# Performance work log

Hardware: AMD Instinct MI355X
Metric: run time of the kernel (lower is better)

The kernel has to match this reference:

```python
import jax, jax.numpy as jnp
import numpy as np

GRID_SIZE = 5   # efficient-kan default
K = 3           # spline_order
BATCH = 32768
OBS_DIM = 128
ACTION_DIM = 18
# (in_features, out_features) for the 7 KANLinear layers:
# base: 128->256->256->64 ; adv head: 64->64->18 ; value head: 64->64->1
DIMS = [(OBS_DIM, 256), (256, 256), (256, 64), (64, 64), (64, ACTION_DIM), (64, 64), (64, 1)]


def make_grid(in_f):
    # uniform grid on [-1,1] extended by K knots each side: shape (in_f, GRID_SIZE+2K+1)
    h = 2.0 / GRID_SIZE
    g = jnp.arange(-K, GRID_SIZE + K + 1, dtype=jnp.float32) * h - 1.0
    return jnp.broadcast_to(g, (in_f, g.shape[0]))


def b_splines(x, grid):
    # Cox-de Boor recursion; x: (B, in) -> bases (B, in, GRID_SIZE+K)
    xe = x[:, :, None]
    b = ((xe >= grid[:, :-1]) & (xe < grid[:, 1:])).astype(x.dtype)
    for j in range(1, K + 1):
        left = (xe - grid[:, : -(j + 1)]) / (grid[:, j:-1] - grid[:, : -(j + 1)])
        right = (grid[:, j + 1:] - xe) / (grid[:, j + 1:] - grid[:, 1:-j])
        b = left * b[:, :, :-1] + right * b[:, :, 1:]
    return b


def kan_layer(x, bw, sw, sc):
    # efficient-kan KANLinear: silu base path + spline path with standalone scaler
    grid = make_grid(x.shape[1])
    base = jax.nn.silu(x) @ bw.T                              # (B, out)
    bases = b_splines(x, grid)                                # (B, in, G+K)
    spline = jnp.einsum('big,oig->bo', bases, sw * sc[:, :, None])
    return base + spline


def setup_inputs() -> dict:
    key = jax.random.key(0)
    ks = jax.random.split(key, 1 + 3 * len(DIMS))
    inp = {"x": jax.random.normal(ks[0], (BATCH, OBS_DIM), dtype=jnp.float32)}
    for i, (fin, fout) in enumerate(DIMS):
        inp[f"bw{i}"] = jax.random.normal(ks[1 + 3 * i], (fout, fin), dtype=jnp.float32) / np.sqrt(fin).astype(np.float32)
        inp[f"sw{i}"] = jax.random.normal(ks[2 + 3 * i], (fout, fin, GRID_SIZE + K), dtype=jnp.float32) * (0.1 / np.sqrt(fin).astype(np.float32))
        inp[f"sc{i}"] = 1.0 + 0.1 * jax.random.normal(ks[3 + 3 * i], (fout, fin), dtype=jnp.float32)
    return inp


def reference(x, bw0, sw0, sc0, bw1, sw1, sc1, bw2, sw2, sc2,
              bw3, sw3, sc3, bw4, sw4, sc4, bw5, sw5, sc5, bw6, sw6, sc6):
    h = x
    for bw, sw, sc in [(bw0, sw0, sc0), (bw1, sw1, sc1), (bw2, sw2, sc2)]:
        h = kan_layer(h, bw, sw, sc)
    advantage = kan_layer(kan_layer(h, bw3, sw3, sc3), bw4, sw4, sc4)
    state_value = kan_layer(kan_layer(h, bw5, sw5, sc5), bw6, sw6, sc6)
    return (advantage, state_value)
```

## Files before the change

### kernel.cpp

```cpp
#include <hip/hip_runtime.h>

typedef unsigned short u16;
typedef unsigned int   u32;
typedef unsigned long long u64;
typedef __bf16 bf16;
typedef float f32x4  __attribute__((ext_vector_type(4)));
typedef bf16  bf16x8 __attribute__((ext_vector_type(8)));

__device__ __forceinline__ float bf2f(u16 u){ return (float)__builtin_bit_cast(bf16,u); }
__device__ __forceinline__ u16   f2bf(float f){ return __builtin_bit_cast(u16,(bf16)f); }
__device__ __forceinline__ u32   pkbf(float a,float b){ return (u32)f2bf(a)|((u32)f2bf(b)<<16); }

#define NROWS 32768

__device__ __forceinline__ void expand_vals(float x, u32& spk, uint4& bpk)
{
  float s = x * (1.0f/(1.0f+__expf(-x)));
  u16 uh = f2bf(s);
  u16 ul = f2bf(s - bf2f(uh));
  spk = (u32)uh | ((u32)ul<<16);
  float tp = __fmaf_rn(x, 2.5f, 5.5f);
  float fi = floorf(tp);
  float uu = tp - fi;
  float u2=uu*uu, u3=u2*uu, w1=1.0f-uu;
  const float c6 = 0.16666666666666666f;
  float d0 = w1*w1*w1*c6;
  float d1 = (4.0f-6.0f*u2+3.0f*u3)*c6;
  float d2 = (1.0f+3.0f*uu+3.0f*u2-3.0f*u3)*c6;
  float d3 = u3*c6;
  u64 dpk = (u64)pkbf(d0,d1) | ((u64)pkbf(d2,d3)<<32);
  int i0 = (int)fminf(fmaxf(fi,-20.f),20.f);
  int ss = (i0-3)*16;
  u64 A  = dpk << (ss & 63);
  u64 Bv = dpk >> ((64-ss) & 63);
  u64 Cv = dpk << ((ss-64) & 63);
  u64 Dv = dpk >> ((-ss) & 63);
  u64 lo = (ss>=0 && ss<64) ? A : ((ss<0 && ss>-64) ? Dv : 0ull);
  u64 hi = (ss>=64 && ss<128) ? Cv : ((ss>0 && ss<64) ? Bv : 0ull);
  bpk.x=(u32)lo; bpk.y=(u32)(lo>>32); bpk.z=(u32)hi; bpk.w=(u32)(hi>>32);
}

struct PrepArgs {
  const float* bw[7]; const float* sw[7]; const float* sc[7];
  u16* w[7];
  int cin[7]; int coutr[7]; int ntsh[7];
  u32 elems[7];
};

__global__ __launch_bounds__(256) void prep_kernel(PrepArgs pa)
{
  u32 idx = blockIdx.x*256 + threadIdx.x;
  int L = 0;
  u32 off = idx;
  while (L < 6 && off >= pa.elems[L]) { off -= pa.elems[L]; ++L; }
  int j    = off & 7;
  int lane = (off>>3) & 63;
  u32 tl   = off >> 9;
  int ntsh = pa.ntsh[L];
  u32 kstep = tl >> ntsh;
  int ntile = (int)(tl & ((1u<<ntsh)-1u));
  int o    = ntile*16 + (lane&15);
  int kpos = (lane>>4)*8 + j;
  u32 c = kstep / 5u;
  int r = (int)(kstep - c*5u);
  int i, g; bool sil;
  if (r == 0){ i = (int)c*16 + (kpos>>1);          g = 0;        sil = true;  }
  else       { int kl=(r-1)*32+kpos; i=(int)c*16+(kl>>3); g=kl&7; sil = false; }
  float v = 0.f;
  if (o < pa.coutr[L]) {
    size_t e = (size_t)o*pa.cin[L] + i;
    v = sil ? pa.bw[L][e] : pa.sw[L][e*8+g]*pa.sc[L][e];
  }
  pa.w[L][off] = f2bf(v);
}

template<int CIN,int COUT,int IN_MODE,int OUT_MODE>
__global__ __launch_bounds__(512,4) void kan_layer(const void* __restrict__ hin_,
    const u16* __restrict__ W, void* __restrict__ hout_)
{
  constexpr int NCH = CIN/16;
  constexpr int TOTK = NCH*5;
  constexpr int NTILES = COUT/16;
  constexpr int NT = (COUT>=128)? COUT/128 : 1;
  constexpr int SROW=20, BROW=68, BOFF=64*SROW;
  constexpr int CHUNK = BOFF + 64*BROW;
  __shared__ u32 buf[2][CHUNK];

  const int b0 = blockIdx.x*64;
  const int tid = threadIdx.x;
  const int wave = tid>>6, lane = tid&63, m = lane&15, quad = lane>>4;

  const u16*   __restrict__ hb = (const u16*)hin_;
  const float* __restrict__ hf = (const float*)hin_;

  f32x4 acc[4][NT];
#pragma unroll
  for (int a=0;a<4;++a)
#pragma unroll
    for (int n=0;n<NT;++n) acc[a][n]=(f32x4){0.f,0.f,0.f,0.f};

  bf16x8 bbuf[3][NT];
  auto loadB = [&](int kstep, bf16x8* dst){
    if (kstep < TOTK){
#pragma unroll
      for (int nt=0; nt<NT; ++nt)
        dst[nt] = *(const bf16x8*)(W + (((size_t)kstep*NTILES + ((wave*NT+nt)&(NTILES-1)))*64 + lane)*8);
    }
  };
  loadB(0, bbuf[0]); loadB(1, bbuf[1]);

  float xb[2][2];
  auto loadX = [&](int kc, float* dst){
#pragma unroll
    for (int t=0;t<2;++t){
      int task = t*512+tid, row = task>>4, f = task&15;
      int gi = (b0+row)*CIN + kc*16 + f;
      dst[t] = (IN_MODE==0)? hf[gi] : bf2f(hb[gi]);
    }
  };
  auto expandChunk = [&](const float* xc, u32* dstb){
#pragma unroll
    for (int t=0;t<2;++t){
      int task=t*512+tid, row=task>>4, f=task&15;
      u32 spk; uint4 bpk;
      expand_vals(xc[t], spk, bpk);
      dstb[row*SROW + f] = spk;
      *(uint4*)&dstb[BOFF + row*BROW + f*4] = bpk;
    }
  };

  loadX(0, xb[0]);
  expandChunk(xb[0], buf[0]);
  loadX(1, xb[1]);
  __syncthreads();

  for (int kc=0; kc<NCH; ++kc){
    u32* cur = buf[kc&1];
    u32* nxt = buf[(kc+1)&1];
    if (kc+1 < NCH) expandChunk(xb[(kc+1)&1], nxt);
    if (kc+2 < NCH) loadX(kc+2, xb[kc&1]);
#pragma unroll
    for (int ks=0; ks<5; ++ks){
      const int kstep = kc*5 + ks;
      loadB(kstep+2, bbuf[2]);
      bf16x8 af[4];
#pragma unroll
      for (int mt=0; mt<4; ++mt){
        int row = mt*16 + m;
        af[mt] = (ks==0)
          ? *(const bf16x8*)&cur[row*SROW + quad*4]
          : *(const bf16x8*)&cur[BOFF + row*BROW + (ks-1)*16 + quad*4];
      }
#pragma unroll
      for (int nt=0; nt<NT; ++nt)
#pragma unroll
        for (int mt=0; mt<4; ++mt)
          acc[mt][nt] = __builtin_amdgcn_mfma_f32_16x16x32_bf16(af[mt], bbuf[0][nt], acc[mt][nt],0,0,0);
#pragma unroll
      for (int nt=0; nt<NT; ++nt){ bbuf[0][nt]=bbuf[1][nt]; bbuf[1][nt]=bbuf[2][nt]; }
    }
    __syncthreads();
  }

  if (wave*NT < NTILES){
#pragma unroll
    for (int mt=0; mt<4; ++mt)
#pragma unroll
      for (int nt=0; nt<NT; ++nt)
#pragma unroll
        for (int r=0; r<4; ++r){
          size_t off = (size_t)(b0 + mt*16 + quad*4 + r)*COUT + ((wave*NT+nt)&(NTILES-1))*16 + m;
          if constexpr (OUT_MODE==0) ((float*)hout_)[off] = acc[mt][nt][r];
          else                       ((u16*)hout_)[off]   = f2bf(acc[mt][nt][r]);
        }
  }
}

template<int IN_MODE>
__global__ __launch_bounds__(512,4) void tail_kernel(const void* __restrict__ h2_,
  const u16* __restrict__ W3, const u16* __restrict__ W4,
  const u16* __restrict__ W5, const u16* __restrict__ W6,
  float* __restrict__ out_adv, float* __restrict__ out_val)
{
  constexpr int SROW=20, BROW=68, BOFF=64*20;
  __shared__ u32   Aexp[BOFF + 64*BROW];
  __shared__ float hA[64*65], hV[64*65];

  const int b0 = blockIdx.x*64;
  const int tid = threadIdx.x;
  const int wave = tid>>6, lane = tid&63, m = lane&15, quad = lane>>4;
  const int rg = wave>>2, cg = wave&3;

  const u16*   __restrict__ hb = (const u16*)h2_;
  const float* __restrict__ hf = (const float*)h2_;

  f32x4 a3[2], a5[2];
#pragma unroll
  for (int mt=0;mt<2;++mt){ a3[mt]=(f32x4){0,0,0,0}; a5[mt]=(f32x4){0,0,0,0}; }

  bf16x8 w3b[3], w5b[3];
  auto loadB2 = [&](int kstep, int d){
    if (kstep < 20){
      size_t bi = (((size_t)kstep*4 + cg)*64 + lane)*8;
      w3b[d] = *(const bf16x8*)(W3+bi);
      w5b[d] = *(const bf16x8*)(W5+bi);
    }
  };
  loadB2(0,0); loadB2(1,1);

  float xb[2][2];
  auto loadX = [&](int kc, float* dst){
#pragma unroll
    for (int t=0;t<2;++t){
      int task = t*512+tid, row=task>>4, f=task&15;
      int gi = (b0+row)*64 + kc*16 + f;
      dst[t] = (IN_MODE==0)? hf[gi] : bf2f(hb[gi]);
    }
  };
  loadX(0, xb[0]);

  for (int kc=0; kc<4; ++kc){
    const float* xc = xb[kc&1];
#pragma unroll
    for (int t=0;t<2;++t){
      int task=t*512+tid, row=task>>4, f=task&15;
      u32 spk; uint4 bpk;
      expand_vals(xc[t], spk, bpk);
      Aexp[row*SROW + f] = spk;
      *(uint4*)&Aexp[BOFF + row*BROW + f*4] = bpk;
    }
    if (kc+1 < 4) loadX(kc+1, xb[(kc+1)&1]);
    __syncthreads();
#pragma unroll
    for (int ks=0; ks<5; ++ks){
      const int kstep = kc*5 + ks;
      loadB2(kstep+2, 2);
      bf16x8 af[2];
#pragma unroll
      for (int mt=0; mt<2; ++mt){
        int row = rg*32 + mt*16 + m;
        af[mt] = (ks==0)
          ? *(const bf16x8*)&Aexp[row*SROW + quad*4]
          : *(const bf16x8*)&Aexp[BOFF + row*BROW + (ks-1)*16 + quad*4];
      }
#pragma unroll
      for (int mt=0; mt<2; ++mt){
        a3[mt] = __builtin_amdgcn_mfma_f32_16x16x32_bf16(af[mt], w3b[0], a3[mt],0,0,0);
        a5[mt] = __builtin_amdgcn_mfma_f32_16x16x32_bf16(af[mt], w5b[0], a5[mt],0,0,0);
      }
      w3b[0]=w3b[1]; w3b[1]=w3b[2]; w5b[0]=w5b[1]; w5b[1]=w5b[2];
    }
    __syncthreads();
  }
#pragma unroll
  for (int mt=0;mt<2;++mt)
#pragma unroll
    for (int r=0;r<4;++r){
      int row = rg*32 + mt*16 + quad*4 + r;
      hA[row*65 + cg*16 + m] = a3[mt][r];
      hV[row*65 + cg*16 + m] = a5[mt][r];
    }
  __syncthreads();

  f32x4 a4[2];
#pragma unroll
  for (int mt=0;mt<2;++mt) a4[mt]=(f32x4){0,0,0,0};
  bf16x8 w4b[3];
  auto loadB4 = [&](int kstep, int d){
    if (kstep < 20) w4b[d] = *(const bf16x8*)(W4 + (((size_t)kstep*4 + cg)*64 + lane)*8);
  };
  loadB4(0,0); loadB4(1,1);
  for (int kc=0; kc<4; ++kc){
#pragma unroll
    for (int t=0;t<2;++t){
      int task=t*512+tid, row=task>>4, f=task&15;
      u32 spk; uint4 bpk;
      expand_vals(hA[row*65 + kc*16 + f], spk, bpk);
      Aexp[row*SROW + f] = spk;
      *(uint4*)&Aexp[BOFF + row*BROW + f*4] = bpk;
    }
    __syncthreads();
#pragma unroll
    for (int ks=0; ks<5; ++ks){
      loadB4(kc*5+ks+2, 2);
      bf16x8 af[2];
#pragma unroll
      for (int mt=0; mt<2; ++mt){
        int row = rg*32 + mt*16 + m;
        af[mt] = (ks==0)
          ? *(const bf16x8*)&Aexp[row*SROW + quad*4]
          : *(const bf16x8*)&Aexp[BOFF + row*BROW + (ks-1)*16 + quad*4];
      }
#pragma unroll
      for (int mt=0; mt<2; ++mt)
        a4[mt] = __builtin_amdgcn_mfma_f32_16x16x32_bf16(af[mt], w4b[0], a4[mt],0,0,0);
      w4b[0]=w4b[1]; w4b[1]=w4b[2];
    }
    __syncthreads();
  }
  {
    int col = cg*16 + m;
    if (col < 18){
#pragma unroll
      for (int mt=0;mt<2;++mt)
#pragma unroll
        for (int r=0;r<4;++r)
          out_adv[(size_t)(b0 + rg*32 + mt*16 + quad*4 + r)*18 + col] = a4[mt][r];
    }
  }

  f32x4 a6[2];
#pragma unroll
  for (int mt=0;mt<2;++mt) a6[mt]=(f32x4){0,0,0,0};
  bf16x8 w6b[3];
  auto loadB6 = [&](int kstep, int d){
    if (kstep < 20) w6b[d] = *(const bf16x8*)(W6 + (((size_t)kstep*4 + cg)*64 + lane)*8);
  };
  loadB6(0,0); loadB6(1,1);
  for (int kc=0; kc<4; ++kc){
#pragma unroll
    for (int t=0;t<2;++t){
      int task=t*512+tid, row=task>>4, f=task&15;
      u32 spk; uint4 bpk;
      expand_vals(hV[row*65 + kc*16 + f], spk, bpk);
      Aexp[row*SROW + f] = spk;
      *(uint4*)&Aexp[BOFF + row*BROW + f*4] = bpk;
    }
    __syncthreads();
#pragma unroll
    for (int ks=0; ks<5; ++ks){
      loadB6(kc*5+ks+2, 2);
      bf16x8 af[2];
#pragma unroll
      for (int mt=0; mt<2; ++mt){
        int row = rg*32 + mt*16 + m;
        af[mt] = (ks==0)
          ? *(const bf16x8*)&Aexp[row*SROW + quad*4]
          : *(const bf16x8*)&Aexp[BOFF + row*BROW + (ks-1)*16 + quad*4];
      }
#pragma unroll
      for (int mt=0; mt<2; ++mt)
        a6[mt] = __builtin_amdgcn_mfma_f32_16x16x32_bf16(af[mt], w6b[0], a6[mt],0,0,0);
      w6b[0]=w6b[1]; w6b[1]=w6b[2];
    }
    __syncthreads();
  }
  if (cg==0 && m==0){
#pragma unroll
    for (int mt=0;mt<2;++mt)
#pragma unroll
      for (int r=0;r<4;++r)
        out_val[b0 + rg*32 + mt*16 + quad*4 + r] = a6[mt][r];
  }
}

extern "C" void kernel_launch(void* const* d_in, const int* in_sizes, int n_in,
                              void* d_out, int out_size, void* d_ws, size_t ws_size,
                              hipStream_t stream)
{
  (void)in_sizes; (void)n_in; (void)out_size;
  char* ws = (char*)d_ws;

  const size_t wbytes[7] = {655360u, 1310720u, 327680u, 81920u, 81920u, 81920u, 81920u};
  const bool midf32 = ws_size >= 78118912u;

  u16* W[7];
  char *h0, *h1, *h2;
  if (midf32) {
    h0 = ws;
    h1 = h0 + 33554432u;
    h2 = h1 + 33554432u;
    size_t off = 75497472u;
    for (int l=0;l<7;++l){ W[l] = (u16*)(ws+off); off += wbytes[l]; }
  } else {
    h0 = ws;
    h1 = h0 + 16777216u;
    h2 = h1 + 16777216u;
    size_t off = 37748736u;
    for (int l=0;l<7;++l){ W[l] = (u16*)(ws+off); off += wbytes[l]; }
  }

  PrepArgs pa;
  const int cins[7]   = {128,256,256,64,64,64,64};
  const int coutr[7]  = {256,256,64,64,18,64,1};
  const int ntsh[7]   = {4,4,2,2,2,2,2};
  const u32 elems[7]  = {327680u,655360u,163840u,40960u,40960u,40960u,40960u};
  for (int l=0;l<7;++l){
    pa.bw[l] = (const float*)d_in[1+3*l];
    pa.sw[l] = (const float*)d_in[2+3*l];
    pa.sc[l] = (const float*)d_in[3+3*l];
    pa.w[l]  = W[l];
    pa.cin[l]=cins[l]; pa.coutr[l]=coutr[l]; pa.ntsh[l]=ntsh[l];
    pa.elems[l]=elems[l];
  }
  prep_kernel<<<5120, 256, 0, stream>>>(pa);

  dim3 g(NROWS/64), b(512);
  float* out_adv = (float*)d_out;
  float* out_val = (float*)d_out + (size_t)NROWS*18;
  if (midf32) {
    kan_layer<128,256,0,0><<<g,b,0,stream>>>(d_in[0], W[0], h0);
    kan_layer<256,256,0,0><<<g,b,0,stream>>>(h0, W[1], h1);
    kan_layer<256, 64,0,0><<<g,b,0,stream>>>(h1, W[2], h2);
    tail_kernel<0><<<g,b,0,stream>>>(h2, W[3], W[4], W[5], W[6], out_adv, out_val);
  } else {
    kan_layer<128,256,0,1><<<g,b,0,stream>>>(d_in[0], W[0], h0);
    kan_layer<256,256,1,1><<<g,b,0,stream>>>(h0, W[1], h1);
    kan_layer<256, 64,1,1><<<g,b,0,stream>>>(h1, W[2], h2);
    tail_kernel<1><<<g,b,0,stream>>>(h2, W[3], W[4], W[5], W[6], out_adv, out_val);
  }
}
```

Before: 238.7 us.

## Drop split-bf16 silu term in main layers to shrink K from 10 to 9 per input

The three main KAN layers previously stored silu as a hi/lo bf16 pair, giving 10 K-columns per input feature (2 silu plus 8 spline). They now keep a single bf16 silu value and process 32 input features per chunk, so K drops to 9 per feature and there are fewer MFMA steps. The 1/6 spline constant moves into the prepped weights, and the cubic basis is computed with fewer operations by clamping tp before the floor. The cost is lower silu precision in the main layers, and the larger LDS buffer (BROW 132) may reduce occupancy.

```diff
diff --git a/kernel.cpp b/kernel.cpp
--- a/kernel.cpp
+++ b/kernel.cpp
@@ -13,37 +13,47 @@
 
 #define NROWS 32768
 
-__device__ __forceinline__ void expand_vals(float x, u32& spk, uint4& bpk)
+__device__ __forceinline__ uint4 basis_pk(float x)
+{
+  float tp  = __fmaf_rn(x, 2.5f, 5.5f);
+  float tpc = fminf(fmaxf(tp, -1.0f), 12.0f);
+  float fi  = floorf(tpc);
+  float uu  = tpc - fi;
+  int   i0  = (int)fi;
+  float u2 = uu*uu, u3 = u2*uu, w1 = 1.0f-uu, w2 = w1*w1, w3 = w2*w1;
+  float d1 = __fmaf_rn(3.0f, u3, __fmaf_rn(-6.0f, u2, 4.0f));
+  float d2 = __fmaf_rn(3.0f, w3, __fmaf_rn(-6.0f, w2, 4.0f));
+  u64 dpk = (u64)pkbf(w3, d1) | ((u64)pkbf(d2, u3) << 32);
+  int ss = i0*16 - 48;
+  u64 A  = dpk << (ss & 63);
+  u64 Bv = dpk >> ((64-ss) & 63);
+  u64 Cv = dpk << ((ss-64) & 63);
+  u64 Dv = dpk >> ((-ss) & 63);
+  u64 lo = (ss>=0 && ss<64)   ? A  : ((ss<0 && ss>-64) ? Dv : 0ull);
+  u64 hi = (ss>=64 && ss<128) ? Cv : ((ss>0 && ss<64)  ? Bv : 0ull);
+  uint4 r; r.x=(u32)lo; r.y=(u32)(lo>>32); r.z=(u32)hi; r.w=(u32)(hi>>32);
+  return r;
+}
+
+__device__ __forceinline__ void expand9(float x, u16& sil, uint4& bpk)
+{
+  float s = x * (1.0f/(1.0f+__expf(-x)));
+  sil = f2bf(s);
+  bpk = basis_pk(x);
+}
+__device__ __forceinline__ void expand10(float x, u32& spk, uint4& bpk)
 {
   float s = x * (1.0f/(1.0f+__expf(-x)));
   u16 uh = f2bf(s);
   u16 ul = f2bf(s - bf2f(uh));
   spk = (u32)uh | ((u32)ul<<16);
-  float tp = __fmaf_rn(x, 2.5f, 5.5f);
-  float fi = floorf(tp);
-  float uu = tp - fi;
-  float u2=uu*uu, u3=u2*uu, w1=1.0f-uu;
-  const float c6 = 0.16666666666666666f;
-  float d0 = w1*w1*w1*c6;
-  float d1 = (4.0f-6.0f*u2+3.0f*u3)*c6;
-  float d2 = (1.0f+3.0f*uu+3.0f*u2-3.0f*u3)*c6;
-  float d3 = u3*c6;
-  u64 dpk = (u64)pkbf(d0,d1) | ((u64)pkbf(d2,d3)<<32);
-  int i0 = (int)fminf(fmaxf(fi,-20.f),20.f);
-  int ss = (i0-3)*16;
-  u64 A  = dpk << (ss & 63);
-  u64 Bv = dpk >> ((64-ss) & 63);
-  u64 Cv = dpk << ((ss-64) & 63);
-  u64 Dv = dpk >> ((-ss) & 63);
-  u64 lo = (ss>=0 && ss<64) ? A : ((ss<0 && ss>-64) ? Dv : 0ull);
-  u64 hi = (ss>=64 && ss<128) ? Cv : ((ss>0 && ss<64) ? Bv : 0ull);
-  bpk.x=(u32)lo; bpk.y=(u32)(lo>>32); bpk.z=(u32)hi; bpk.w=(u32)(hi>>32);
+  bpk = basis_pk(x);
 }
 
 struct PrepArgs {
   const float* bw[7]; const float* sw[7]; const float* sc[7];
   u16* w[7];
-  int cin[7]; int coutr[7]; int ntsh[7];
+  int cin[7]; int coutr[7]; int ntsh[7]; int fmt[7];
   u32 elems[7];
 };
 
@@ -61,15 +71,20 @@
   int ntile = (int)(tl & ((1u<<ntsh)-1u));
   int o    = ntile*16 + (lane&15);
   int kpos = (lane>>4)*8 + j;
-  u32 c = kstep / 5u;
-  int r = (int)(kstep - c*5u);
-  int i, g; bool sil;
-  if (r == 0){ i = (int)c*16 + (kpos>>1);          g = 0;        sil = true;  }
-  else       { int kl=(r-1)*32+kpos; i=(int)c*16+(kl>>3); g=kl&7; sil = false; }
+  int i = 0, g = 0; bool sil;
+  if (pa.fmt[L] == 0){
+    u32 c = kstep/9u; int r = (int)(kstep - c*9u);
+    if (r == 0){ i = (int)c*32 + kpos; sil = true; }
+    else { int kl=(r-1)*32+kpos; i=(int)c*32+(kl>>3); g=kl&7; sil = false; }
+  } else {
+    u32 c = kstep/5u; int r = (int)(kstep - c*5u);
+    if (r == 0){ i = (int)c*16 + (kpos>>1); sil = true; }
+    else { int kl=(r-1)*32+kpos; i=(int)c*16+(kl>>3); g=kl&7; sil = false; }
+  }
   float v = 0.f;
   if (o < pa.coutr[L]) {
     size_t e = (size_t)o*pa.cin[L] + i;
-    v = sil ? pa.bw[L][e] : pa.sw[L][e*8+g]*pa.sc[L][e];
+    v = sil ? pa.bw[L][e] : pa.sw[L][e*8+g]*pa.sc[L][e]*0.16666666666666666f;
   }
   pa.w[L][off] = f2bf(v);
 }
@@ -78,11 +93,11 @@
 __global__ __launch_bounds__(512,4) void kan_layer(const void* __restrict__ hin_,
     const u16* __restrict__ W, void* __restrict__ hout_)
 {
-  constexpr int NCH = CIN/16;
-  constexpr int TOTK = NCH*5;
+  constexpr int NCH = CIN/32;
+  constexpr int TOTK = NCH*9;
   constexpr int NTILES = COUT/16;
   constexpr int NT = (COUT>=128)? COUT/128 : 1;
-  constexpr int SROW=20, BROW=68, BOFF=64*SROW;
+  constexpr int SROW=20, BROW=132, BOFF=64*SROW;
   constexpr int CHUNK = BOFF + 64*BROW;
   __shared__ u32 buf[2][CHUNK];
 
@@ -109,29 +124,29 @@
   };
   loadB(0, bbuf[0]); loadB(1, bbuf[1]);
 
-  float xb[2][2];
+  float xb[2][4];
   auto loadX = [&](int kc, float* dst){
 #pragma unroll
-    for (int t=0;t<2;++t){
-      int task = t*512+tid, row = task>>4, f = task&15;
-      int gi = (b0+row)*CIN + kc*16 + f;
+    for (int t=0;t<4;++t){
+      int task = t*512+tid, row = task>>5, f = task&31;
+      int gi = (b0+row)*CIN + kc*32 + f;
       dst[t] = (IN_MODE==0)? hf[gi] : bf2f(hb[gi]);
     }
   };
   auto expandChunk = [&](const float* xc, u32* dstb){
 #pragma unroll
-    for (int t=0;t<2;++t){
-      int task=t*512+tid, row=task>>4, f=task&15;
-      u32 spk; uint4 bpk;
-      expand_vals(xc[t], spk, bpk);
-      dstb[row*SROW + f] = spk;
+    for (int t=0;t<4;++t){
+      int task=t*512+tid, row=task>>5, f=task&31;
+      u16 sil; uint4 bpk;
+      expand9(xc[t], sil, bpk);
+      ((u16*)dstb)[row*(SROW*2) + f] = sil;
       *(uint4*)&dstb[BOFF + row*BROW + f*4] = bpk;
     }
   };
 
   loadX(0, xb[0]);
   expandChunk(xb[0], buf[0]);
-  loadX(1, xb[1]);
+  if (NCH > 1) loadX(1, xb[1]);
   __syncthreads();
 
   for (int kc=0; kc<NCH; ++kc){
@@ -140,8 +155,8 @@
     if (kc+1 < NCH) expandChunk(xb[(kc+1)&1], nxt);
     if (kc+2 < NCH) loadX(kc+2, xb[kc&1]);
 #pragma unroll
-    for (int ks=0; ks<5; ++ks){
-      const int kstep = kc*5 + ks;
+    for (int ks=0; ks<9; ++ks){
+      const int kstep = kc*9 + ks;
       loadB(kstep+2, bbuf[2]);
       bf16x8 af[4];
 #pragma unroll
@@ -225,7 +240,7 @@
     for (int t=0;t<2;++t){
       int task=t*512+tid, row=task>>4, f=task&15;
       u32 spk; uint4 bpk;
-      expand_vals(xc[t], spk, bpk);
+      expand10(xc[t], spk, bpk);
       Aexp[row*SROW + f] = spk;
       *(uint4*)&Aexp[BOFF + row*BROW + f*4] = bpk;
     }
@@ -275,7 +290,7 @@
     for (int t=0;t<2;++t){
       int task=t*512+tid, row=task>>4, f=task&15;
       u32 spk; uint4 bpk;
-      expand_vals(hA[row*65 + kc*16 + f], spk, bpk);
+      expand10(hA[row*65 + kc*16 + f], spk, bpk);
       Aexp[row*SROW + f] = spk;
       *(uint4*)&Aexp[BOFF + row*BROW + f*4] = bpk;
     }
@@ -322,7 +337,7 @@
     for (int t=0;t<2;++t){
       int task=t*512+tid, row=task>>4, f=task&15;
       u32 spk; uint4 bpk;
-      expand_vals(hV[row*65 + kc*16 + f], spk, bpk);
+      expand10(hV[row*65 + kc*16 + f], spk, bpk);
       Aexp[row*SROW + f] = spk;
       *(uint4*)&Aexp[BOFF + row*BROW + f*4] = bpk;
     }
@@ -361,8 +376,8 @@
   (void)in_sizes; (void)n_in; (void)out_size;
   char* ws = (char*)d_ws;
 
-  const size_t wbytes[7] = {655360u, 1310720u, 327680u, 81920u, 81920u, 81920u, 81920u};
-  const bool midf32 = ws_size >= 78118912u;
+  const size_t wbytes[7] = {589824u, 1179648u, 294912u, 81920u, 81920u, 81920u, 81920u};
+  const bool midf32 = ws_size >= 77889536u;
 
   u16* W[7];
   char *h0, *h1, *h2;
@@ -384,16 +399,17 @@
   const int cins[7]   = {128,256,256,64,64,64,64};
   const int coutr[7]  = {256,256,64,64,18,64,1};
   const int ntsh[7]   = {4,4,2,2,2,2,2};
-  const u32 elems[7]  = {327680u,655360u,163840u,40960u,40960u,40960u,40960u};
+  const int fmts[7]   = {0,0,0,1,1,1,1};
+  const u32 elems[7]  = {294912u,589824u,147456u,40960u,40960u,40960u,40960u};
   for (int l=0;l<7;++l){
     pa.bw[l] = (const float*)d_in[1+3*l];
     pa.sw[l] = (const float*)d_in[2+3*l];
     pa.sc[l] = (const float*)d_in[3+3*l];
     pa.w[l]  = W[l];
-    pa.cin[l]=cins[l]; pa.coutr[l]=coutr[l]; pa.ntsh[l]=ntsh[l];
+    pa.cin[l]=cins[l]; pa.coutr[l]=coutr[l]; pa.ntsh[l]=ntsh[l]; pa.fmt[l]=fmts[l];
     pa.elems[l]=elems[l];
   }
-  prep_kernel<<<5120, 256, 0, stream>>>(pa);
+  prep_kernel<<<4672, 256, 0, stream>>>(pa);
 
   dim3 g(NROWS/64), b(512);
   float* out_adv = (float*)d_out;
```

Result: faster. 231.1 us (-3.2%).
